# Optimization experiments

Measured on AMD Instinct MI355X. Metric: run time of the kernel, lower is better.

The kernel has to match this reference:

```python
import jax, jax.numpy as jnp
import numpy as np

DIM = 768
HEADS = 12
HEAD_DIM = DIM // HEADS
EPS = 1e-5


def setup_inputs() -> dict:
    key = jax.random.key(0)
    ks = jax.random.split(key, 9)
    s = 0.02
    x = jax.random.normal(ks[0], (4, 1024, DIM), dtype=jnp.float32)
    return {
        "x": x,
        "Wqkv_c": jax.random.normal(ks[1], (DIM, 3 * DIM), jnp.float32) * s,
        "bqkv_c": jnp.zeros((3 * DIM,), jnp.float32),
        "Wp_c": jax.random.normal(ks[2], (DIM, DIM), jnp.float32) * s,
        "bp_c": jnp.zeros((DIM,), jnp.float32),
        "Wqkv_ac": jax.random.normal(ks[3], (DIM, 3 * DIM), jnp.float32) * s,
        "bqkv_ac": jnp.zeros((3 * DIM,), jnp.float32),
        "Wp_ac": jax.random.normal(ks[4], (DIM, DIM), jnp.float32) * s,
        "bp_ac": jnp.zeros((DIM,), jnp.float32),
        "gamma": jnp.ones((DIM,), jnp.float32),
        "beta": jnp.zeros((DIM,), jnp.float32),
    }


def _branch(x, Wqkv, bqkv, Wp, bp, causal: bool):
    B, T, C = x.shape
    qkv = (x @ Wqkv + bqkv).reshape(B, T, 3, HEADS, HEAD_DIM)
    qkv = jnp.transpose(qkv, (2, 0, 3, 1, 4))  # [3,B,H,T,Dh]
    q, k, v = qkv[0], qkv[1], qkv[2]
    scores = jnp.einsum("bhqd,bhkd->bhqk", q, k) / np.sqrt(HEAD_DIM).astype(np.float32)
    i = jnp.arange(T)[:, None]
    j = jnp.arange(T)[None, :]
    mask = (j <= i) if causal else (j >= i)  # tril / triu (incl. diagonal)
    scores = jnp.where(mask[None, None], scores, -jnp.inf)
    attn = jax.nn.softmax(scores, axis=-1)
    out = jnp.einsum("bhqk,bhkd->bhqd", attn, v)
    out = jnp.transpose(out, (0, 2, 1, 3)).reshape(B, T, C)
    return out @ Wp + bp


def reference(x, Wqkv_c, bqkv_c, Wp_c, bp_c, Wqkv_ac, bqkv_ac, Wp_ac, bp_ac, gamma, beta):
    out_c = _branch(x, Wqkv_c, bqkv_c, Wp_c, bp_c, causal=True)
    out_ac = _branch(x, Wqkv_ac, bqkv_ac, Wp_ac, bp_ac, causal=False)
    y = x + out_c + out_ac  # residual; dropout is identity at eval
    mu = jnp.mean(y, axis=-1, keepdims=True)
    var = jnp.var(y, axis=-1, keepdims=True)
    return (y - mu) * jax.lax.rsqrt(var + EPS) * gamma + beta
```

## Files before the change

### kernel.cpp

```cpp
#include <hip/hip_runtime.h>
#include <stdint.h>

#define DIM 768
#define HEADS 12
#define HD 64
#define BATCH 4
#define SEQ 1024
#define NTOK (BATCH*SEQ)
#define QKVW (3*DIM)
#define QKW (2*DIM)
#define EPS 1e-5f

typedef __attribute__((ext_vector_type(8))) short short8;
typedef __attribute__((ext_vector_type(4))) float f32x4;

__device__ __forceinline__ unsigned short f2bf(float f) {
    union { float f; unsigned u; } v; v.f = f;
    unsigned r = v.u + 0x7fffu + ((v.u >> 16) & 1u);
    return (unsigned short)(r >> 16);
}

__device__ __forceinline__ void gld_lds16(const void* g, void* l) {
    auto gp = reinterpret_cast<const __attribute__((address_space(1))) unsigned int*>(
        (uintptr_t)g);
    auto lp = reinterpret_cast<__attribute__((address_space(3))) unsigned int*>(
        (unsigned int)(uintptr_t)l);
    __builtin_amdgcn_global_load_lds(gp, lp, 16, 0, 0);
}

__global__ __launch_bounds__(256) void cvt_kernel(
    const float* __restrict__ in, unsigned short* __restrict__ out)
{
    const int i = blockIdx.x * 256 + threadIdx.x;
    const float4 v = ((const float4*)in)[i];
    ushort4 o4;
    o4.x = f2bf(v.x); o4.y = f2bf(v.y); o4.z = f2bf(v.z); o4.w = f2bf(v.w);
    ((ushort4*)out)[i] = o4;
}

__global__ __launch_bounds__(256) void cvtT_kernel(
    const float* __restrict__ W0, const float* __restrict__ W1,
    unsigned short* __restrict__ T0, unsigned short* __restrict__ T1,
    const int K, const int N)
{
    const float* __restrict__ W = blockIdx.z ? W1 : W0;
    unsigned short* __restrict__ WT = blockIdx.z ? T1 : T0;
    __shared__ float t[32][33];
    const int n0 = blockIdx.x * 32, k0 = blockIdx.y * 32;
    const int c = threadIdx.x & 31, rr = threadIdx.x >> 5;
#pragma unroll
    for (int i = 0; i < 4; ++i)
        t[rr + 8 * i][c] = W[(size_t)(k0 + rr + 8 * i) * N + n0 + c];
    __syncthreads();
#pragma unroll
    for (int i = 0; i < 4; ++i)
        WT[(size_t)(n0 + rr + 8 * i) * K + k0 + c] = f2bf(t[c][rr + 8 * i]);
}

__global__ __launch_bounds__(256) void gemm_qkv_kernel(
    const unsigned short* __restrict__ A,
    const unsigned short* __restrict__ BT0, const unsigned short* __restrict__ BT1,
    const float* __restrict__ bias0, const float* __restrict__ bias1,
    unsigned short* __restrict__ QK0, unsigned short* __restrict__ QK1,
    unsigned short* __restrict__ VT0, unsigned short* __restrict__ VT1)
{
    const int z = blockIdx.z;
    const unsigned short* __restrict__ BT = z ? BT1 : BT0;
    const float* __restrict__ bias = z ? bias1 : bias0;
    unsigned short* __restrict__ QK = z ? QK1 : QK0;
    unsigned short* __restrict__ VT = z ? VT1 : VT0;
    const int K = DIM;

    __shared__ __align__(16) unsigned short Als[128 * 32];
    __shared__ __align__(16) unsigned short Bls[128 * 32];
    const int tid = threadIdx.x, lane = tid & 63, wv = tid >> 6;
    const int m0 = blockIdx.y * 128, n0 = blockIdx.x * 128;
    const int wr = wv >> 1, wc = wv & 1;
    const int fm = lane & 15, fk = (lane >> 4) * 8;
    const int c0 = wv * 2;
    const int arow = c0 * 16 + (lane >> 2), kk = (lane & 3) * 8;

    f32x4 acc[4][4];
#pragma unroll
    for (int i = 0; i < 4; ++i)
#pragma unroll
        for (int j = 0; j < 4; ++j) acc[i][j] = f32x4{0.f, 0.f, 0.f, 0.f};

    for (int k0 = 0; k0 < K; k0 += 32) {
        gld_lds16(A  + (size_t)(m0 + arow)      * K + k0 + kk, &Als[c0 * 512]);
        gld_lds16(A  + (size_t)(m0 + arow + 16) * K + k0 + kk, &Als[c0 * 512 + 512]);
        gld_lds16(BT + (size_t)(n0 + arow)      * K + k0 + kk, &Bls[c0 * 512]);
        gld_lds16(BT + (size_t)(n0 + arow + 16) * K + k0 + kk, &Bls[c0 * 512 + 512]);
        __syncthreads();
        short8 af[4], bf[4];
#pragma unroll
        for (int i = 0; i < 4; ++i)
            af[i] = *(const short8*)&Als[(wr * 64 + i * 16 + fm) * 32 + fk];
#pragma unroll
        for (int j = 0; j < 4; ++j)
            bf[j] = *(const short8*)&Bls[(wc * 64 + j * 16 + fm) * 32 + fk];
#pragma unroll
        for (int i = 0; i < 4; ++i)
#pragma unroll
            for (int j = 0; j < 4; ++j)
                acc[i][j] = __builtin_amdgcn_mfma_f32_16x16x32_bf16(af[i], bf[j], acc[i][j], 0, 0, 0);
        __syncthreads();
    }
    const int rbase = (lane >> 4) * 4;
    if (n0 < QKW) {
        const float qsc = (n0 < DIM) ? 0.125f : 1.0f;
#pragma unroll
        for (int i = 0; i < 4; ++i) {
            const int m = m0 + wr * 64 + i * 16 + rbase;
#pragma unroll
            for (int j = 0; j < 4; ++j) {
                const int n = n0 + wc * 64 + j * 16 + fm;
                const float bs = bias[n];
#pragma unroll
                for (int r = 0; r < 4; ++r)
                    QK[(size_t)(m + r) * QKW + n] = f2bf((acc[i][j][r] + bs) * qsc);
            }
        }
    } else {
#pragma unroll
        for (int i = 0; i < 4; ++i) {
            const int m = m0 + wr * 64 + i * 16 + rbase;
            const int b = m >> 10, t = m & 1023;
#pragma unroll
            for (int j = 0; j < 4; ++j) {
                const int n = n0 + wc * 64 + j * 16 + fm;
                const int nh = n - QKW;
                const float bs = bias[n];
                const unsigned p0 = f2bf(acc[i][j][0] + bs);
                const unsigned p1 = f2bf(acc[i][j][1] + bs);
                const unsigned p2 = f2bf(acc[i][j][2] + bs);
                const unsigned p3 = f2bf(acc[i][j][3] + bs);
                uint2 u; u.x = p0 | (p1 << 16); u.y = p2 | (p3 << 16);
                *(uint2*)(VT + ((size_t)((b * HEADS + (nh >> 6)) * HD + (nh & 63)) * SEQ + t)) = u;
            }
        }
    }
}

__global__ __launch_bounds__(256) void gemm_proj_kernel(
    const unsigned short* __restrict__ A0, const unsigned short* __restrict__ BT0,
    const unsigned short* __restrict__ A1, const unsigned short* __restrict__ BT1,
    const float* __restrict__ b0, const float* __restrict__ b1,
    const float* __restrict__ xres, float* __restrict__ Y)
{
    __shared__ __align__(16) unsigned short Als[128 * 32];
    __shared__ __align__(16) unsigned short Bls[128 * 32];
    const int tid = threadIdx.x, lane = tid & 63, wv = tid >> 6;
    const int m0 = blockIdx.y * 128, n0 = blockIdx.x * 128;
    const int wr = wv >> 1, wc = wv & 1;
    const int fm = lane & 15, fk = (lane >> 4) * 8;
    const int c0 = wv * 2;
    const int arow = c0 * 16 + (lane >> 2), kk = (lane & 3) * 8;
    const int K = DIM;

    f32x4 acc[4][4];
#pragma unroll
    for (int i = 0; i < 4; ++i)
#pragma unroll
        for (int j = 0; j < 4; ++j) acc[i][j] = f32x4{0.f, 0.f, 0.f, 0.f};

#pragma unroll
    for (int ph = 0; ph < 2; ++ph) {
        const unsigned short* __restrict__ A  = ph ? A1 : A0;
        const unsigned short* __restrict__ BT = ph ? BT1 : BT0;
        for (int k0 = 0; k0 < K; k0 += 32) {
            gld_lds16(A  + (size_t)(m0 + arow)      * K + k0 + kk, &Als[c0 * 512]);
            gld_lds16(A  + (size_t)(m0 + arow + 16) * K + k0 + kk, &Als[c0 * 512 + 512]);
            gld_lds16(BT + (size_t)(n0 + arow)      * K + k0 + kk, &Bls[c0 * 512]);
            gld_lds16(BT + (size_t)(n0 + arow + 16) * K + k0 + kk, &Bls[c0 * 512 + 512]);
            __syncthreads();
            short8 af[4], bf[4];
#pragma unroll
            for (int i = 0; i < 4; ++i)
                af[i] = *(const short8*)&Als[(wr * 64 + i * 16 + fm) * 32 + fk];
#pragma unroll
            for (int j = 0; j < 4; ++j)
                bf[j] = *(const short8*)&Bls[(wc * 64 + j * 16 + fm) * 32 + fk];
#pragma unroll
            for (int i = 0; i < 4; ++i)
#pragma unroll
                for (int j = 0; j < 4; ++j)
                    acc[i][j] = __builtin_amdgcn_mfma_f32_16x16x32_bf16(af[i], bf[j], acc[i][j], 0, 0, 0);
            __syncthreads();
        }
    }
    const int rbase = (lane >> 4) * 4;
#pragma unroll
    for (int i = 0; i < 4; ++i) {
        const int m = m0 + wr * 64 + i * 16 + rbase;
#pragma unroll
        for (int j = 0; j < 4; ++j) {
            const int n = n0 + wc * 64 + j * 16 + fm;
            const float bs = b0[n] + b1[n];
#pragma unroll
            for (int r = 0; r < 4; ++r) {
                const size_t idx = (size_t)(m + r) * DIM + n;
                Y[idx] = acc[i][j][r] + xres[idx] + bs;
            }
        }
    }
}

#define KP 72
__global__ __launch_bounds__(256, 3) void attn_fused_kernel(
    const unsigned short* __restrict__ qk_c, const unsigned short* __restrict__ vT_c,
    const unsigned short* __restrict__ qk_ac, const unsigned short* __restrict__ vT_ac,
    unsigned short* __restrict__ o_c, unsigned short* __restrict__ o_ac)
{
    __shared__ __align__(16) unsigned short Kls[64 * KP];
    __shared__ __align__(16) unsigned short Vls[64 * KP];
    __shared__ __align__(16) unsigned short Ps[4][16 * KP];
    const int tid = threadIdx.x, lane = tid & 63, w = tid >> 6;
    const int fm = lane & 15, fg = lane >> 4;
    const int bh = blockIdx.x, qt = blockIdx.y;
    const int b = bh / HEADS, h = bh % HEADS;
    unsigned short* Psw = &Ps[w][0];
    const int srow = tid >> 3, sseg = (tid & 7) * 8;

    for (int br = 0; br < 2; ++br) {
        const int causal = (br == 0);
        const unsigned short* __restrict__ qk = causal ? qk_c : qk_ac;
        const unsigned short* __restrict__ vT = causal ? vT_c : vT_ac;
        unsigned short* __restrict__ o = causal ? o_c : o_ac;
        const unsigned short* qbase = qk + (size_t)b * SEQ * QKW + h * HD;
        const unsigned short* kbase = qbase + DIM;
        const unsigned short* vtb   = vT + (size_t)(b * HEADS + h) * HD * SEQ;

        short8 qb0, qb1;
        {
            const size_t qoff = (size_t)(qt * 64 + w * 16 + fm) * QKW + fg * 8;
            qb0 = *(const short8*)(qbase + qoff);
            qb1 = *(const short8*)(qbase + qoff + 32);
        }

        float ls = 0.f;
        f32x4 accO[4];
#pragma unroll
        for (int dj = 0; dj < 4; ++dj) accO[dj] = f32x4{0.f, 0.f, 0.f, 0.f};

        const int ktb = causal ? 0 : qt;
        const int kte = causal ? qt : (SEQ / 64 - 1);

        for (int kt = ktb; kt <= kte; ++kt) {
            uint4 kr0, kr1, vr0, vr1;
            {
                const int r0 = srow, r1 = srow + 32;
                kr0 = *(const uint4*)(kbase + (size_t)(kt * 64 + r0) * QKW + sseg);
                kr1 = *(const uint4*)(kbase + (size_t)(kt * 64 + r1) * QKW + sseg);
                vr0 = *(const uint4*)(vtb + (size_t)r0 * SEQ + kt * 64 + sseg);
                vr1 = *(const uint4*)(vtb + (size_t)r1 * SEQ + kt * 64 + sseg);
            }
            __syncthreads();
            *(uint4*)(&Kls[srow * KP + sseg])        = kr0;
            *(uint4*)(&Kls[(srow + 32) * KP + sseg]) = kr1;
            *(uint4*)(&Vls[srow * KP + sseg])        = vr0;
            *(uint4*)(&Vls[(srow + 32) * KP + sseg]) = vr1;
            __syncthreads();

            f32x4 st[4];
#pragma unroll
            for (int kj = 0; kj < 4; ++kj) {
                const short8 ka0 = *(const short8*)&Kls[(kj * 16 + fm) * KP + fg * 8];
                const short8 ka1 = *(const short8*)&Kls[(kj * 16 + fm) * KP + 32 + fg * 8];
                st[kj] = __builtin_amdgcn_mfma_f32_16x16x32_bf16(ka0, qb0, f32x4{0.f,0.f,0.f,0.f}, 0, 0, 0);
                st[kj] = __builtin_amdgcn_mfma_f32_16x16x32_bf16(ka1, qb1, st[kj], 0, 0, 0);
            }
            const bool diag = (kt == qt);
#pragma unroll
            for (int kj = 0; kj < 4; ++kj) {
                float e[4];
#pragma unroll
                for (int r = 0; r < 4; ++r) {
                    float v = st[kj][r];
                    if (diag) {
                        const int ki = kj * 16 + fg * 4 + r;
                        const int qi = w * 16 + fm;
                        const bool ok = causal ? (ki <= qi) : (ki >= qi);
                        if (!ok) v = -1e30f;
                    }
                    e[r] = __expf(v);
                    ls += e[r];
                }
                const unsigned p0 = f2bf(e[0]);
                const unsigned p1 = f2bf(e[1]);
                const unsigned p2 = f2bf(e[2]);
                const unsigned p3 = f2bf(e[3]);
                uint2 u; u.x = p0 | (p1 << 16); u.y = p2 | (p3 << 16);
                *(uint2*)(Psw + fm * KP + kj * 16 + fg * 4) = u;
            }
            const short8 ap0 = *(const short8*)(Psw + fm * KP + fg * 8);
            const short8 ap1 = *(const short8*)(Psw + fm * KP + 32 + fg * 8);
#pragma unroll
            for (int dj = 0; dj < 4; ++dj) {
                const short8 vb0 = *(const short8*)&Vls[(dj * 16 + fm) * KP + fg * 8];
                const short8 vb1 = *(const short8*)&Vls[(dj * 16 + fm) * KP + 32 + fg * 8];
                accO[dj] = __builtin_amdgcn_mfma_f32_16x16x32_bf16(ap0, vb0, accO[dj], 0, 0, 0);
                accO[dj] = __builtin_amdgcn_mfma_f32_16x16x32_bf16(ap1, vb1, accO[dj], 0, 0, 0);
            }
        }

        float lt = ls;
        lt += __shfl_xor(lt, 16);
        lt += __shfl_xor(lt, 32);
        float li_o[4];
#pragma unroll
        for (int r = 0; r < 4; ++r) li_o[r] = __shfl(lt, fg * 4 + r);
#pragma unroll
        for (int r = 0; r < 4; ++r) {
            const float inv = 1.f / li_o[r];
            const int q = qt * 64 + w * 16 + fg * 4 + r;
            unsigned short* orow = o + ((size_t)b * SEQ + q) * DIM + h * HD;
#pragma unroll
            for (int dj = 0; dj < 4; ++dj)
                orow[dj * 16 + fm] = f2bf(accO[dj][r] * inv);
        }
    }
}

__global__ __launch_bounds__(256) void ln_kernel(
    const float* __restrict__ Y, const float* __restrict__ gamma,
    const float* __restrict__ beta, float* __restrict__ out)
{
    const int row = blockIdx.x;
    const int tid = threadIdx.x;
    const float* yr = Y + (size_t)row * DIM;
    float v0 = yr[tid], v1 = yr[tid + 256], v2 = yr[tid + 512];
    float s = v0 + v1 + v2;
    float q = v0 * v0 + v1 * v1 + v2 * v2;
#pragma unroll
    for (int off = 32; off > 0; off >>= 1) {
        s += __shfl_down(s, off);
        q += __shfl_down(q, off);
    }
    __shared__ float rs_[4], rq_[4];
    const int wv = tid >> 6;
    if ((tid & 63) == 0) { rs_[wv] = s; rq_[wv] = q; }
    __syncthreads();
    const float ts = rs_[0] + rs_[1] + rs_[2] + rs_[3];
    const float tq = rq_[0] + rq_[1] + rq_[2] + rq_[3];
    const float mu = ts * (1.f / DIM);
    const float var = tq * (1.f / DIM) - mu * mu;
    const float rstd = rsqrtf(var + EPS);
    out[(size_t)row * DIM + tid]       = (v0 - mu) * rstd * gamma[tid]       + beta[tid];
    out[(size_t)row * DIM + tid + 256] = (v1 - mu) * rstd * gamma[tid + 256] + beta[tid + 256];
    out[(size_t)row * DIM + tid + 512] = (v2 - mu) * rstd * gamma[tid + 512] + beta[tid + 512];
}

extern "C" void kernel_launch(void* const* d_in, const int* in_sizes, int n_in,
                              void* d_out, int out_size, void* d_ws, size_t ws_size,
                              hipStream_t stream)
{
    const float* x       = (const float*)d_in[0];
    const float* Wqkv_c  = (const float*)d_in[1];
    const float* bqkv_c  = (const float*)d_in[2];
    const float* Wp_c    = (const float*)d_in[3];
    const float* bp_c    = (const float*)d_in[4];
    const float* Wqkv_ac = (const float*)d_in[5];
    const float* bqkv_ac = (const float*)d_in[6];
    const float* Wp_ac   = (const float*)d_in[7];
    const float* bp_ac   = (const float*)d_in[8];
    const float* gamma   = (const float*)d_in[9];
    const float* beta    = (const float*)d_in[10];
    float* out = (float*)d_out;

    char* p = (char*)d_ws;
    unsigned short* qk_c   = (unsigned short*)p; p += (size_t)NTOK * QKW * 2;
    unsigned short* qk_ac  = (unsigned short*)p; p += (size_t)NTOK * QKW * 2;
    unsigned short* vT_c   = (unsigned short*)p; p += (size_t)NTOK * DIM * 2;
    unsigned short* vT_ac  = (unsigned short*)p; p += (size_t)NTOK * DIM * 2;
    unsigned short* o_ac   = (unsigned short*)p; p += (size_t)NTOK * DIM * 2;
    unsigned short* xb     = (unsigned short*)p; p += (size_t)NTOK * DIM * 2;
    unsigned short* WqT_c  = (unsigned short*)p; p += (size_t)QKVW * DIM * 2;
    unsigned short* WqT_ac = (unsigned short*)p; p += (size_t)QKVW * DIM * 2;
    unsigned short* WpT_c  = (unsigned short*)p; p += (size_t)DIM * DIM * 2;
    unsigned short* WpT_ac = (unsigned short*)p; p += (size_t)DIM * DIM * 2;
    unsigned short* o_c = WqT_c;
    float*          Y   = (float*)vT_c;

    cvt_kernel<<<NTOK * DIM / 1024, 256, 0, stream>>>(x, xb);
    cvtT_kernel<<<dim3(QKVW / 32, DIM / 32, 2), 256, 0, stream>>>(
        Wqkv_c, Wqkv_ac, WqT_c, WqT_ac, DIM, QKVW);
    cvtT_kernel<<<dim3(DIM / 32, DIM / 32, 2), 256, 0, stream>>>(
        Wp_c, Wp_ac, WpT_c, WpT_ac, DIM, DIM);

    gemm_qkv_kernel<<<dim3(QKVW / 128, NTOK / 128, 2), 256, 0, stream>>>(
        xb, WqT_c, WqT_ac, bqkv_c, bqkv_ac, qk_c, qk_ac, vT_c, vT_ac);

    attn_fused_kernel<<<dim3(BATCH * HEADS, SEQ / 64), 256, 0, stream>>>(
        qk_c, vT_c, qk_ac, vT_ac, o_c, o_ac);

    gemm_proj_kernel<<<dim3(DIM / 128, NTOK / 128), 256, 0, stream>>>(
        o_c, WpT_c, o_ac, WpT_ac, bp_c, bp_ac, x, Y);
    ln_kernel<<<NTOK, 256, 0, stream>>>(Y, gamma, beta, out);
}
```

Before: 230.2 us.

## Double-buffer LDS tiles in GEMMs and attention, split projection GEMM by branch

Adds double-buffered shared-memory tiles to the QKV GEMM, the projection GEMM and the attention kernel, so the next tile's loads are issued before the current tile's MFMAs and one barrier per iteration is removed. The projection GEMM no longer accumulates both branches serially in one block. It now uses 64-row tiles with a z dimension per branch, which raises the grid from 192 to 768 blocks, and writes two partial outputs that the layernorm kernel sums. The cost is double the LDS use, which may lower occupancy, plus an extra fp32 intermediate write and read.

```diff
diff --git a/kernel.cpp b/kernel.cpp
--- a/kernel.cpp
+++ b/kernel.cpp
@@ -71,8 +71,8 @@
     unsigned short* __restrict__ VT = z ? VT1 : VT0;
     const int K = DIM;
 
-    __shared__ __align__(16) unsigned short Als[128 * 32];
-    __shared__ __align__(16) unsigned short Bls[128 * 32];
+    __shared__ __align__(16) unsigned short Als[2][128 * 32];
+    __shared__ __align__(16) unsigned short Bls[2][128 * 32];
     const int tid = threadIdx.x, lane = tid & 63, wv = tid >> 6;
     const int m0 = blockIdx.y * 128, n0 = blockIdx.x * 128;
     const int wr = wv >> 1, wc = wv & 1;
@@ -80,31 +80,45 @@
     const int c0 = wv * 2;
     const int arow = c0 * 16 + (lane >> 2), kk = (lane & 3) * 8;
 
+    const unsigned short* Ag0 = A  + (size_t)(m0 + arow)      * K + kk;
+    const unsigned short* Ag1 = A  + (size_t)(m0 + arow + 16) * K + kk;
+    const unsigned short* Bg0 = BT + (size_t)(n0 + arow)      * K + kk;
+    const unsigned short* Bg1 = BT + (size_t)(n0 + arow + 16) * K + kk;
+
     f32x4 acc[4][4];
 #pragma unroll
     for (int i = 0; i < 4; ++i)
 #pragma unroll
         for (int j = 0; j < 4; ++j) acc[i][j] = f32x4{0.f, 0.f, 0.f, 0.f};
 
-    for (int k0 = 0; k0 < K; k0 += 32) {
-        gld_lds16(A  + (size_t)(m0 + arow)      * K + k0 + kk, &Als[c0 * 512]);
-        gld_lds16(A  + (size_t)(m0 + arow + 16) * K + k0 + kk, &Als[c0 * 512 + 512]);
-        gld_lds16(BT + (size_t)(n0 + arow)      * K + k0 + kk, &Bls[c0 * 512]);
-        gld_lds16(BT + (size_t)(n0 + arow + 16) * K + k0 + kk, &Bls[c0 * 512 + 512]);
+    gld_lds16(Ag0, &Als[0][c0 * 512]);
+    gld_lds16(Ag1, &Als[0][c0 * 512 + 512]);
+    gld_lds16(Bg0, &Bls[0][c0 * 512]);
+    gld_lds16(Bg1, &Bls[0][c0 * 512 + 512]);
+
+    const int NK = K / 32;
+    for (int kt = 0; kt < NK; ++kt) {
+        const int p = kt & 1;
         __syncthreads();
+        if (kt + 1 < NK) {
+            const int off = (kt + 1) * 32;
+            gld_lds16(Ag0 + off, &Als[p ^ 1][c0 * 512]);
+            gld_lds16(Ag1 + off, &Als[p ^ 1][c0 * 512 + 512]);
+            gld_lds16(Bg0 + off, &Bls[p ^ 1][c0 * 512]);
+            gld_lds16(Bg1 + off, &Bls[p ^ 1][c0 * 512 + 512]);
+        }
         short8 af[4], bf[4];
 #pragma unroll
         for (int i = 0; i < 4; ++i)
-            af[i] = *(const short8*)&Als[(wr * 64 + i * 16 + fm) * 32 + fk];
+            af[i] = *(const short8*)&Als[p][(wr * 64 + i * 16 + fm) * 32 + fk];
 #pragma unroll
         for (int j = 0; j < 4; ++j)
-            bf[j] = *(const short8*)&Bls[(wc * 64 + j * 16 + fm) * 32 + fk];
+            bf[j] = *(const short8*)&Bls[p][(wc * 64 + j * 16 + fm) * 32 + fk];
 #pragma unroll
         for (int i = 0; i < 4; ++i)
 #pragma unroll
             for (int j = 0; j < 4; ++j)
                 acc[i][j] = __builtin_amdgcn_mfma_f32_16x16x32_bf16(af[i], bf[j], acc[i][j], 0, 0, 0);
-        __syncthreads();
     }
     const int rbase = (lane >> 4) * 4;
     if (n0 < QKW) {
@@ -146,61 +160,73 @@
     const unsigned short* __restrict__ A0, const unsigned short* __restrict__ BT0,
     const unsigned short* __restrict__ A1, const unsigned short* __restrict__ BT1,
     const float* __restrict__ b0, const float* __restrict__ b1,
-    const float* __restrict__ xres, float* __restrict__ Y)
-{
-    __shared__ __align__(16) unsigned short Als[128 * 32];
-    __shared__ __align__(16) unsigned short Bls[128 * 32];
+    const float* __restrict__ xres, float* __restrict__ Y0, float* __restrict__ Y1)
+{
+    const int z = blockIdx.z;
+    const unsigned short* __restrict__ A  = z ? A1 : A0;
+    const unsigned short* __restrict__ BT = z ? BT1 : BT0;
+    __shared__ __align__(16) unsigned short Als[2][64 * 32];
+    __shared__ __align__(16) unsigned short Bls[2][128 * 32];
     const int tid = threadIdx.x, lane = tid & 63, wv = tid >> 6;
-    const int m0 = blockIdx.y * 128, n0 = blockIdx.x * 128;
-    const int wr = wv >> 1, wc = wv & 1;
-    const int fm = lane & 15, fk = (lane >> 4) * 8;
-    const int c0 = wv * 2;
-    const int arow = c0 * 16 + (lane >> 2), kk = (lane & 3) * 8;
+    const int m0 = blockIdx.y * 64, n0 = blockIdx.x * 128;
+    const int fm = lane & 15, fg = lane >> 4, fk = (lane >> 4) * 8;
+    const int srw = lane >> 2, kk = (lane & 3) * 8;
     const int K = DIM;
 
-    f32x4 acc[4][4];
+    const unsigned short* Ag  = A  + (size_t)(m0 + wv * 16 + srw) * K + kk;
+    const unsigned short* Bg0 = BT + (size_t)(n0 + wv * 32 + srw) * K + kk;
+    const unsigned short* Bg1 = BT + (size_t)(n0 + wv * 32 + 16 + srw) * K + kk;
+
+    f32x4 acc[4][2];
 #pragma unroll
     for (int i = 0; i < 4; ++i)
 #pragma unroll
-        for (int j = 0; j < 4; ++j) acc[i][j] = f32x4{0.f, 0.f, 0.f, 0.f};
-
-#pragma unroll
-    for (int ph = 0; ph < 2; ++ph) {
-        const unsigned short* __restrict__ A  = ph ? A1 : A0;
-        const unsigned short* __restrict__ BT = ph ? BT1 : BT0;
-        for (int k0 = 0; k0 < K; k0 += 32) {
-            gld_lds16(A  + (size_t)(m0 + arow)      * K + k0 + kk, &Als[c0 * 512]);
-            gld_lds16(A  + (size_t)(m0 + arow + 16) * K + k0 + kk, &Als[c0 * 512 + 512]);
-            gld_lds16(BT + (size_t)(n0 + arow)      * K + k0 + kk, &Bls[c0 * 512]);
-            gld_lds16(BT + (size_t)(n0 + arow + 16) * K + k0 + kk, &Bls[c0 * 512 + 512]);
-            __syncthreads();
-            short8 af[4], bf[4];
-#pragma unroll
-            for (int i = 0; i < 4; ++i)
-                af[i] = *(const short8*)&Als[(wr * 64 + i * 16 + fm) * 32 + fk];
-#pragma unroll
-            for (int j = 0; j < 4; ++j)
-                bf[j] = *(const short8*)&Bls[(wc * 64 + j * 16 + fm) * 32 + fk];
-#pragma unroll
-            for (int i = 0; i < 4; ++i)
-#pragma unroll
-                for (int j = 0; j < 4; ++j)
-                    acc[i][j] = __builtin_amdgcn_mfma_f32_16x16x32_bf16(af[i], bf[j], acc[i][j], 0, 0, 0);
-            __syncthreads();
-        }
-    }
-    const int rbase = (lane >> 4) * 4;
+        for (int j = 0; j < 2; ++j) acc[i][j] = f32x4{0.f, 0.f, 0.f, 0.f};
+
+    gld_lds16(Ag,  &Als[0][wv * 512]);
+    gld_lds16(Bg0, &Bls[0][wv * 1024]);
+    gld_lds16(Bg1, &Bls[0][wv * 1024 + 512]);
+
+    const int NK = K / 32;
+    for (int kt = 0; kt < NK; ++kt) {
+        const int p = kt & 1;
+        __syncthreads();
+        if (kt + 1 < NK) {
+            const int off = (kt + 1) * 32;
+            gld_lds16(Ag + off,  &Als[p ^ 1][wv * 512]);
+            gld_lds16(Bg0 + off, &Bls[p ^ 1][wv * 1024]);
+            gld_lds16(Bg1 + off, &Bls[p ^ 1][wv * 1024 + 512]);
+        }
+        short8 af[4], bf[2];
+#pragma unroll
+        for (int i = 0; i < 4; ++i)
+            af[i] = *(const short8*)&Als[p][(i * 16 + fm) * 32 + fk];
+#pragma unroll
+        for (int j = 0; j < 2; ++j)
+            bf[j] = *(const short8*)&Bls[p][(wv * 32 + j * 16 + fm) * 32 + fk];
+#pragma unroll
+        for (int i = 0; i < 4; ++i)
+#pragma unroll
+            for (int j = 0; j < 2; ++j)
+                acc[i][j] = __builtin_amdgcn_mfma_f32_16x16x32_bf16(af[i], bf[j], acc[i][j], 0, 0, 0);
+    }
 #pragma unroll
     for (int i = 0; i < 4; ++i) {
-        const int m = m0 + wr * 64 + i * 16 + rbase;
-#pragma unroll
-        for (int j = 0; j < 4; ++j) {
-            const int n = n0 + wc * 64 + j * 16 + fm;
-            const float bs = b0[n] + b1[n];
-#pragma unroll
-            for (int r = 0; r < 4; ++r) {
-                const size_t idx = (size_t)(m + r) * DIM + n;
-                Y[idx] = acc[i][j][r] + xres[idx] + bs;
+        const int m = m0 + i * 16 + fg * 4;
+#pragma unroll
+        for (int j = 0; j < 2; ++j) {
+            const int n = n0 + wv * 32 + j * 16 + fm;
+            if (z == 0) {
+                const float bs = b0[n] + b1[n];
+#pragma unroll
+                for (int r = 0; r < 4; ++r) {
+                    const size_t idx = (size_t)(m + r) * DIM + n;
+                    Y0[idx] = acc[i][j][r] + xres[idx] + bs;
+                }
+            } else {
+#pragma unroll
+                for (int r = 0; r < 4; ++r)
+                    Y1[(size_t)(m + r) * DIM + n] = acc[i][j][r];
             }
         }
     }
@@ -212,8 +238,8 @@
     const unsigned short* __restrict__ qk_ac, const unsigned short* __restrict__ vT_ac,
     unsigned short* __restrict__ o_c, unsigned short* __restrict__ o_ac)
 {
-    __shared__ __align__(16) unsigned short Kls[64 * KP];
-    __shared__ __align__(16) unsigned short Vls[64 * KP];
+    __shared__ __align__(16) unsigned short Kls[2][64 * KP];
+    __shared__ __align__(16) unsigned short Vls[2][64 * KP];
     __shared__ __align__(16) unsigned short Ps[4][16 * KP];
     const int tid = threadIdx.x, lane = tid & 63, w = tid >> 6;
     const int fm = lane & 15, fg = lane >> 4;
@@ -246,27 +272,32 @@
         const int ktb = causal ? 0 : qt;
         const int kte = causal ? qt : (SEQ / 64 - 1);
 
+        uint4 kr0 = *(const uint4*)(kbase + (size_t)(ktb * 64 + srow) * QKW + sseg);
+        uint4 kr1 = *(const uint4*)(kbase + (size_t)(ktb * 64 + srow + 32) * QKW + sseg);
+        uint4 vr0 = *(const uint4*)(vtb + (size_t)srow * SEQ + ktb * 64 + sseg);
+        uint4 vr1 = *(const uint4*)(vtb + (size_t)(srow + 32) * SEQ + ktb * 64 + sseg);
+
+        if (br) __syncthreads();
+        int p = 0;
         for (int kt = ktb; kt <= kte; ++kt) {
-            uint4 kr0, kr1, vr0, vr1;
-            {
-                const int r0 = srow, r1 = srow + 32;
-                kr0 = *(const uint4*)(kbase + (size_t)(kt * 64 + r0) * QKW + sseg);
-                kr1 = *(const uint4*)(kbase + (size_t)(kt * 64 + r1) * QKW + sseg);
-                vr0 = *(const uint4*)(vtb + (size_t)r0 * SEQ + kt * 64 + sseg);
-                vr1 = *(const uint4*)(vtb + (size_t)r1 * SEQ + kt * 64 + sseg);
+            *(uint4*)(&Kls[p][srow * KP + sseg])        = kr0;
+            *(uint4*)(&Kls[p][(srow + 32) * KP + sseg]) = kr1;
+            *(uint4*)(&Vls[p][srow * KP + sseg])        = vr0;
+            *(uint4*)(&Vls[p][(srow + 32) * KP + sseg]) = vr1;
+            if (kt < kte) {
+                const int ktn = kt + 1;
+                kr0 = *(const uint4*)(kbase + (size_t)(ktn * 64 + srow) * QKW + sseg);
+                kr1 = *(const uint4*)(kbase + (size_t)(ktn * 64 + srow + 32) * QKW + sseg);
+                vr0 = *(const uint4*)(vtb + (size_t)srow * SEQ + ktn * 64 + sseg);
+                vr1 = *(const uint4*)(vtb + (size_t)(srow + 32) * SEQ + ktn * 64 + sseg);
             }
             __syncthreads();
-            *(uint4*)(&Kls[srow * KP + sseg])        = kr0;
-            *(uint4*)(&Kls[(srow + 32) * KP + sseg]) = kr1;
-            *(uint4*)(&Vls[srow * KP + sseg])        = vr0;
-            *(uint4*)(&Vls[(srow + 32) * KP + sseg]) = vr1;
-            __syncthreads();
 
             f32x4 st[4];
 #pragma unroll
             for (int kj = 0; kj < 4; ++kj) {
-                const short8 ka0 = *(const short8*)&Kls[(kj * 16 + fm) * KP + fg * 8];
-                const short8 ka1 = *(const short8*)&Kls[(kj * 16 + fm) * KP + 32 + fg * 8];
+                const short8 ka0 = *(const short8*)&Kls[p][(kj * 16 + fm) * KP + fg * 8];
+                const short8 ka1 = *(const short8*)&Kls[p][(kj * 16 + fm) * KP + 32 + fg * 8];
                 st[kj] = __builtin_amdgcn_mfma_f32_16x16x32_bf16(ka0, qb0, f32x4{0.f,0.f,0.f,0.f}, 0, 0, 0);
                 st[kj] = __builtin_amdgcn_mfma_f32_16x16x32_bf16(ka1, qb1, st[kj], 0, 0, 0);
             }
@@ -297,11 +328,12 @@
             const short8 ap1 = *(const short8*)(Psw + fm * KP + 32 + fg * 8);
 #pragma unroll
             for (int dj = 0; dj < 4; ++dj) {
-                const short8 vb0 = *(const short8*)&Vls[(dj * 16 + fm) * KP + fg * 8];
-                const short8 vb1 = *(const short8*)&Vls[(dj * 16 + fm) * KP + 32 + fg * 8];
+                const short8 vb0 = *(const short8*)&Vls[p][(dj * 16 + fm) * KP + fg * 8];
+                const short8 vb1 = *(const short8*)&Vls[p][(dj * 16 + fm) * KP + 32 + fg * 8];
                 accO[dj] = __builtin_amdgcn_mfma_f32_16x16x32_bf16(ap0, vb0, accO[dj], 0, 0, 0);
                 accO[dj] = __builtin_amdgcn_mfma_f32_16x16x32_bf16(ap1, vb1, accO[dj], 0, 0, 0);
             }
+            p ^= 1;
         }
 
         float lt = ls;
@@ -323,13 +355,17 @@
 }
 
 __global__ __launch_bounds__(256) void ln_kernel(
-    const float* __restrict__ Y, const float* __restrict__ gamma,
-    const float* __restrict__ beta, float* __restrict__ out)
+    const float* __restrict__ Y0, const float* __restrict__ Y1,
+    const float* __restrict__ gamma, const float* __restrict__ beta,
+    float* __restrict__ out)
 {
     const int row = blockIdx.x;
     const int tid = threadIdx.x;
-    const float* yr = Y + (size_t)row * DIM;
-    float v0 = yr[tid], v1 = yr[tid + 256], v2 = yr[tid + 512];
+    const float* y0r = Y0 + (size_t)row * DIM;
+    const float* y1r = Y1 + (size_t)row * DIM;
+    float v0 = y0r[tid] + y1r[tid];
+    float v1 = y0r[tid + 256] + y1r[tid + 256];
+    float v2 = y0r[tid + 512] + y1r[tid + 512];
     float s = v0 + v1 + v2;
     float q = v0 * v0 + v1 * v1 + v2 * v2;
 #pragma unroll
@@ -380,7 +416,8 @@
     unsigned short* WpT_c  = (unsigned short*)p; p += (size_t)DIM * DIM * 2;
     unsigned short* WpT_ac = (unsigned short*)p; p += (size_t)DIM * DIM * 2;
     unsigned short* o_c = WqT_c;
-    float*          Y   = (float*)vT_c;
+    float*          Y0  = (float*)qk_c;
+    float*          Y1  = (float*)vT_c;
 
     cvt_kernel<<<NTOK * DIM / 1024, 256, 0, stream>>>(x, xb);
     cvtT_kernel<<<dim3(QKVW / 32, DIM / 32, 2), 256, 0, stream>>>(
@@ -394,7 +431,7 @@
     attn_fused_kernel<<<dim3(BATCH * HEADS, SEQ / 64), 256, 0, stream>>>(
         qk_c, vT_c, qk_ac, vT_ac, o_c, o_ac);
 
-    gemm_proj_kernel<<<dim3(DIM / 128, NTOK / 128), 256, 0, stream>>>(
-        o_c, WpT_c, o_ac, WpT_ac, bp_c, bp_ac, x, Y);
-    ln_kernel<<<NTOK, 256, 0, stream>>>(Y, gamma, beta, out);
-}
+    gemm_proj_kernel<<<dim3(DIM / 128, NTOK / 64, 2), 256, 0, stream>>>(
+        o_c, WpT_c, o_ac, WpT_ac, bp_c, bp_ac, x, Y0, Y1);
+    ln_kernel<<<NTOK, 256, 0, stream>>>(Y0, Y1, gamma, beta, out);
+}
```

After: 205.1 us. 10.9% less time.
